# Performance work log

Hardware: AMD Instinct MI355X
Metric: run time of the kernel (lower is better)

Reference implementation:

```python
import jax, jax.numpy as jnp
import numpy as np

D_MODEL = 1024
ED = 2048        # d_inner = expand_factor * d_model
N = 16           # d_state
DT_RANK = 64     # ceil(d_model/16)
K = 4            # d_conv
B_SZ = 4
L = 512


def _causal_depthwise_conv(u, w, b):
    # u: [B, L, ED], w: [ED, 1, K], b: [ED]
    xc = jnp.transpose(u, (0, 2, 1))  # [B, ED, L]
    xc = jax.lax.conv_general_dilated(
        xc, w, window_strides=(1,), padding=[(K - 1, 0)],
        feature_group_count=ED, dimension_numbers=('NCH', 'OIH', 'NCH'))
    xc = xc + b[None, :, None]
    return jnp.transpose(xc, (0, 2, 1))  # [B, L, ED]


def _ssm_branch(xz_half, z, conv_w, conv_b, Wx, Wdt, b_dt, A_log, Dp):
    # xz_half, z: [B, L, ED]
    x = jax.nn.silu(_causal_depthwise_conv(xz_half, conv_w, conv_b))
    dbc = x @ Wx.T  # [B, L, dt_rank + 2N]
    delta = dbc[..., :DT_RANK]
    Bm = dbc[..., DT_RANK:DT_RANK + N]
    Cm = dbc[..., DT_RANK + N:]
    delta = jax.nn.softplus(delta @ Wdt.T + b_dt)  # [B, L, ED]
    A = -jnp.exp(A_log)  # [ED, N]
    dA = jnp.exp(delta[..., None] * A)                        # [B, L, ED, N]
    bx = (delta[..., None] * Bm[:, :, None, :]) * x[..., None]  # [B, L, ED, N]
    dA_t = jnp.transpose(dA, (1, 0, 2, 3))
    bx_t = jnp.transpose(bx, (1, 0, 2, 3))
    c_t = jnp.transpose(Cm, (1, 0, 2))  # [L, B, N]
    h0 = jnp.zeros((x.shape[0], ED, N), dtype=x.dtype)

    def step(h, inp):
        dAi, bxi, ci = inp
        h = dAi * h + bxi
        return h, jnp.einsum('ben,bn->be', h, ci)

    _, ys = jax.lax.scan(step, h0, (dA_t, bx_t, c_t))
    y = jnp.transpose(ys, (1, 0, 2)) + Dp * x  # D skip connection
    return y * jax.nn.silu(z)                  # gate


def _mamba_block(x, W_in, conv_w, conv_b, Wx, Wdt, b_dt, A_log, Dp,
                 conv_w_b, conv_b_b, Wx_b, Wdt_b, b_dt_b, A_log_b, Dp_b, W_out):
    xz = x @ W_in.T  # [B, L, 2*ED]
    xf, zf = xz[..., :ED], xz[..., ED:]
    y = _ssm_branch(xf, zf, conv_w, conv_b, Wx, Wdt, b_dt, A_log, Dp)
    xz_r = xz[:, ::-1, :]
    xb, zb = xz_r[..., :ED], xz_r[..., ED:]
    y_b = _ssm_branch(xb, zb, conv_w_b, conv_b_b, Wx_b, Wdt_b, b_dt_b, A_log_b, Dp_b)
    y = (y + y_b[:, ::-1, :]) * 0.5
    return y @ W_out.T


def setup_inputs() -> dict:
    key = jax.random.key(0)
    ks = jax.random.split(key, 20)
    s = lambda k, shp, sc: jax.random.normal(k, shp, dtype=jnp.float32) * sc
    dt = jnp.exp(jax.random.uniform(ks[15], (ED,)) * (np.log(0.1) - np.log(0.001)) + np.log(0.001))
    dt = jnp.clip(dt, 1e-4, None)
    inv_dt = dt + jnp.log(-jnp.expm1(-dt))
    A_init = jnp.log(jnp.tile(jnp.arange(1, N + 1, dtype=jnp.float32), (ED, 1)))
    return {
        'x': s(ks[0], (B_SZ, L, D_MODEL), 1.0),
        'W_in': s(ks[1], (2 * ED, D_MODEL), D_MODEL ** -0.5),
        'conv_w': s(ks[2], (ED, 1, K), K ** -0.5),
        'conv_b': s(ks[3], (ED,), 0.02),
        'Wx': s(ks[4], (DT_RANK + 2 * N, ED), ED ** -0.5),
        'Wdt': jax.random.uniform(ks[5], (ED, DT_RANK), minval=-DT_RANK ** -0.5, maxval=DT_RANK ** -0.5),
        'b_dt': inv_dt,
        'A_log': A_init,
        'Dp': jnp.ones((ED,), dtype=jnp.float32),
        'conv_w_b': s(ks[6], (ED, 1, K), K ** -0.5),
        'conv_b_b': s(ks[7], (ED,), 0.02),
        'Wx_b': s(ks[8], (DT_RANK + 2 * N, ED), ED ** -0.5),
        'Wdt_b': jax.random.uniform(ks[9], (ED, DT_RANK), minval=-DT_RANK ** -0.5, maxval=DT_RANK ** -0.5),
        'b_dt_b': inv_dt,
        'A_log_b': A_init,
        'Dp_b': jnp.ones((ED,), dtype=jnp.float32),
        'W_out': s(ks[10], (D_MODEL, ED), ED ** -0.5),
    }


def reference(x, W_in, conv_w, conv_b, Wx, Wdt, b_dt, A_log, Dp,
              conv_w_b, conv_b_b, Wx_b, Wdt_b, b_dt_b, A_log_b, Dp_b, W_out):
    return _mamba_block(x, W_in, conv_w, conv_b, Wx, Wdt, b_dt, A_log, Dp,
                        conv_w_b, conv_b_b, Wx_b, Wdt_b, b_dt_b, A_log_b, Dp_b, W_out)
```

## Files before the change

kernel.cpp:

```cpp
#include <hip/hip_runtime.h>
#include <hip/hip_bf16.h>
#include <stdint.h>

typedef unsigned short ushort_t;
typedef __attribute__((ext_vector_type(8))) short short8;
typedef __attribute__((ext_vector_type(4))) float f32x4;
typedef __attribute__((ext_vector_type(2))) float f32x2;

__device__ __forceinline__ float b2f(ushort_t u) {
    union { uint32_t i; float f; } v; v.i = ((uint32_t)u) << 16; return v.f;
}
__device__ __forceinline__ ushort_t f2b(float f) {
    union { float f; uint32_t i; } v; v.f = f;
    uint32_t r = v.i + 0x7fff + ((v.i >> 16) & 1);
    return (ushort_t)(r >> 16);
}

#if __has_builtin(__builtin_amdgcn_exp2f)
#define EXP2(x) __builtin_amdgcn_exp2f(x)
#else
#define EXP2(x) __expf((x) * 0.69314718056f)
#endif

__device__ __forceinline__ void ll16(const ushort_t* g, ushort_t* l) {
    __builtin_amdgcn_global_load_lds(
        (const __attribute__((address_space(1))) uint32_t*)g,
        (__attribute__((address_space(3))) uint32_t*)l, 16, 0, 0);
}

template <int CTRL>
__device__ __forceinline__ float dpp_add(float p) {
    int v = __builtin_amdgcn_update_dpp(0, __float_as_int(p), CTRL, 0xF, 0xF, true);
    return p + __int_as_float(v);
}
#define DPP_XOR1 0xB1
#define DPP_XOR2 0x4E
#define DPP_HMIR 0x141

__device__ __forceinline__ void epi_wave_f32(
    float* sw, const f32x4* accg, float* dst0, int ldc, int lane)
{
    const int quad = lane >> 4, lr = lane & 15;
#pragma unroll
    for (int j = 0; j < 4; j++)
#pragma unroll
        for (int r = 0; r < 4; r++)
            sw[(quad * 4 + r) * 64 + j * 16 + lr] = accg[j][r];
    __asm__ volatile("s_waitcnt lgkmcnt(0)" ::: "memory");
#pragma unroll
    for (int t = 0; t < 4; t++) {
        int row = t * 4 + quad;
        float4 v = *(const float4*)(&sw[row * 64 + lr * 4]);
        *(float4*)(dst0 + (size_t)row * ldc + lr * 4) = v;
    }
}

__device__ __forceinline__ void epi_wave_b16(
    float* sw, const f32x4* accg, ushort_t* dst0, int ldc, int lane)
{
    const int quad = lane >> 4, lr = lane & 15;
#pragma unroll
    for (int j = 0; j < 4; j++)
#pragma unroll
        for (int r = 0; r < 4; r++)
            sw[(quad * 4 + r) * 64 + j * 16 + lr] = accg[j][r];
    __asm__ volatile("s_waitcnt lgkmcnt(0)" ::: "memory");
#pragma unroll
    for (int t = 0; t < 4; t++) {
        int row = t * 4 + quad;
        float4 v = *(const float4*)(&sw[row * 64 + lr * 4]);
        ushort4 o; o.x = f2b(v.x); o.y = f2b(v.y); o.z = f2b(v.z); o.w = f2b(v.w);
        *(ushort4*)(dst0 + (size_t)row * ldc + lr * 4) = o;
    }
}

struct CastSeg { const float4* src; ushort4* dst; };
struct CastArgs { CastSeg seg[7]; int start[8]; };

__global__ __launch_bounds__(256) void cast_multi(CastArgs a)
{
    int g = blockIdx.x * 256 + threadIdx.x;
    if (g >= a.start[7]) return;
    int s = 0;
#pragma unroll
    for (int i = 1; i < 7; i++) s += (g >= a.start[i]);
    int i = g - a.start[s];
    float4 v = a.seg[s].src[i];
    ushort4 o;
    o.x = f2b(v.x); o.y = f2b(v.y); o.z = f2b(v.z); o.w = f2b(v.w);
    a.seg[s].dst[i] = o;
}

#define BK 32

__global__ __launch_bounds__(256) void gemm_g1(
    const ushort_t* __restrict__ A, int lda,
    const ushort_t* __restrict__ B, int ldb,
    ushort_t* __restrict__ Cout, int ldc, int Kd)
{
    __shared__ ushort_t As[2][128 * BK];
    __shared__ ushort_t Bs[2][128 * BK];
    __shared__ float sepi[4][1024];

    const int tid  = threadIdx.x;
    const int m0   = blockIdx.y * 128;
    const int n0   = blockIdx.x * 128;
    const int wv   = tid >> 6;
    const int lane = tid & 63;
    const int wm   = (wv >> 1) * 64;
    const int wn   = (wv & 1) * 64;
    const int lr   = lane & 15;
    const int quad = lane >> 4;

    f32x4 acc[4][4];
#pragma unroll
    for (int i = 0; i < 4; i++)
#pragma unroll
        for (int j = 0; j < 4; j++) acc[i][j] = f32x4{0.f, 0.f, 0.f, 0.f};

    const int srA = wv * 32 + (lane >> 2);
    const int scA = (lane & 3) * 8;

    auto stage = [&](int bf_, int k0) {
        ll16(A + (size_t)(m0 + srA) * lda + k0 + scA,      &As[bf_][wv * 1024]);
        ll16(A + (size_t)(m0 + srA + 16) * lda + k0 + scA, &As[bf_][wv * 1024 + 512]);
        ll16(B + (size_t)(n0 + srA) * ldb + k0 + scA,      &Bs[bf_][wv * 1024]);
        ll16(B + (size_t)(n0 + srA + 16) * ldb + k0 + scA, &Bs[bf_][wv * 1024 + 512]);
    };

    const int nk = Kd / BK;
    stage(0, 0);
    __syncthreads();

    for (int t = 0; t < nk; ++t) {
        const int buf = t & 1;
        if (t + 1 < nk) stage(buf ^ 1, (t + 1) * BK);

        short8 af[4], bfr[4];
#pragma unroll
        for (int i = 0; i < 4; i++)
            af[i] = *(const short8*)(&As[buf][(wm + i * 16 + lr) * BK + quad * 8]);
#pragma unroll
        for (int j = 0; j < 4; j++)
            bfr[j] = *(const short8*)(&Bs[buf][(wn + j * 16 + lr) * BK + quad * 8]);
#pragma unroll
        for (int i = 0; i < 4; i++)
#pragma unroll
            for (int j = 0; j < 4; j++)
                acc[i][j] = __builtin_amdgcn_mfma_f32_16x16x32_bf16(af[i], bfr[j], acc[i][j], 0, 0, 0);
        __syncthreads();
    }

#pragma unroll
    for (int g = 0; g < 4; g++)
        epi_wave_b16(sepi[wv], acc[g],
                     Cout + (size_t)(m0 + wm + g * 16) * ldc + n0 + wn, ldc, lane);
}

__global__ __launch_bounds__(256) void gemm_g4(
    const ushort_t* __restrict__ yfp, const ushort_t* __restrict__ ybp,
    const ushort_t* __restrict__ B, int ldb,
    float* __restrict__ part)
{
    __shared__ ushort_t As[2][64 * BK];
    __shared__ ushort_t Bs[2][128 * BK];
    __shared__ float sepi[4][1024];

    const int tid  = threadIdx.x;
    const int m0   = blockIdx.y * 64;
    const int n0   = blockIdx.x * 128;
    const int kz   = blockIdx.z;
    const int kbase = kz * 1024;
    const int wv   = tid >> 6;
    const int lane = tid & 63;
    const int wm   = (wv >> 1) * 32;
    const int wn   = (wv & 1) * 64;
    const int lr   = lane & 15;
    const int quad = lane >> 4;

    f32x4 acc[2][4];
#pragma unroll
    for (int i = 0; i < 2; i++)
#pragma unroll
        for (int j = 0; j < 4; j++) acc[i][j] = f32x4{0.f, 0.f, 0.f, 0.f};

    const int srA = wv * 16 + (lane >> 2);
    const int srB = wv * 32 + (lane >> 2);
    const int sc  = (lane & 3) * 8;

    const int arow = m0 + srA;
    const int t_   = arow & 511;
    const size_t yf_off = (size_t)arow * 2048;
    const size_t yb_off = (size_t)(arow - t_ + 511 - t_) * 2048;

    uint4 ra, rb;
    auto loadA = [&](int k0) {
        ra = *(const uint4*)(yfp + yf_off + kbase + k0 + sc);
        rb = *(const uint4*)(ybp + yb_off + kbase + k0 + sc);
    };
    auto writeA = [&](int bf_) {
        const uint32_t pa[4] = { ra.x, ra.y, ra.z, ra.w };
        const uint32_t pb[4] = { rb.x, rb.y, rb.z, rb.w };
        uint32_t w[4];
#pragma unroll
        for (int k = 0; k < 4; k++) {
            float a0 = b2f((ushort_t)(pa[k] & 0xffff));
            float a1 = b2f((ushort_t)(pa[k] >> 16));
            float c0 = b2f((ushort_t)(pb[k] & 0xffff));
            float c1 = b2f((ushort_t)(pb[k] >> 16));
            w[k] = (uint32_t)f2b(0.5f * (a0 + c0)) |
                   ((uint32_t)f2b(0.5f * (a1 + c1)) << 16);
        }
        *(uint4*)(&As[bf_][wv * 512 + (lane >> 2) * 32 + (lane & 3) * 8]) =
            make_uint4(w[0], w[1], w[2], w[3]);
    };
    auto stageB = [&](int bf_, int k0) {
        ll16(B + (size_t)(n0 + srB) * ldb + kbase + k0 + sc,      &Bs[bf_][wv * 1024]);
        ll16(B + (size_t)(n0 + srB + 16) * ldb + kbase + k0 + sc, &Bs[bf_][wv * 1024 + 512]);
    };

    const int nk = 1024 / BK;
    loadA(0);
    stageB(0, 0);
    writeA(0);
    __syncthreads();

    for (int t = 0; t < nk; ++t) {
        const int buf = t & 1;
        if (t + 1 < nk) {
            loadA((t + 1) * BK);
            stageB(buf ^ 1, (t + 1) * BK);
        }

        short8 af[2], bfr[4];
#pragma unroll
        for (int i = 0; i < 2; i++)
            af[i] = *(const short8*)(&As[buf][(wm + i * 16 + lr) * BK + quad * 8]);
#pragma unroll
        for (int j = 0; j < 4; j++)
            bfr[j] = *(const short8*)(&Bs[buf][(wn + j * 16 + lr) * BK + quad * 8]);
#pragma unroll
        for (int i = 0; i < 2; i++)
#pragma unroll
            for (int j = 0; j < 4; j++)
                acc[i][j] = __builtin_amdgcn_mfma_f32_16x16x32_bf16(af[i], bfr[j], acc[i][j], 0, 0, 0);

        if (t + 1 < nk) writeA(buf ^ 1);
        __syncthreads();
    }

    float* Cout = part + (size_t)kz * 2048 * 1024;
#pragma unroll
    for (int g = 0; g < 2; g++)
        epi_wave_f32(sepi[wv], acc[g],
                     Cout + (size_t)(m0 + wm + g * 16) * 1024 + n0 + wn, 1024, lane);
}

__global__ __launch_bounds__(256) void reduce_g4(
    const float4* __restrict__ part, float4* __restrict__ out)
{
    int g = blockIdx.x * 256 + threadIdx.x;
    const int S = 2048 * 1024 / 4;
    float4 a = part[g], b = part[g + S];
    float4 o; o.x = a.x + b.x; o.y = a.y + b.y; o.z = a.z + b.z; o.w = a.w + b.w;
    out[g] = o;
}

__global__ __launch_bounds__(256) void gemm_g2(
    const ushort_t* __restrict__ xc, const ushort_t* __restrict__ wx,
    float* __restrict__ part)
{
    __shared__ ushort_t As[2][128 * BK];
    __shared__ ushort_t Bs[2][128 * BK];
    __shared__ float sepi[4][1024];

    const int sk = blockIdx.x, mb = blockIdx.y, br = blockIdx.z;
    const ushort_t* A = xc + (size_t)br * 2048 * 2048;
    const ushort_t* B = wx + (size_t)br * 96 * 2048;
    float* C = part + (size_t)(sk * 2 + br) * 2048 * 96;
    const int m0 = mb * 128;
    const int kb = sk * 256;

    const int tid  = threadIdx.x;
    const int wv   = tid >> 6;
    const int lane = tid & 63;
    const int wm   = (wv >> 1) * 64;
    const int wn   = (wv & 1) * 64;
    const int lr   = lane & 15;
    const int quad = lane >> 4;

    f32x4 acc[4][4];
#pragma unroll
    for (int i = 0; i < 4; i++)
#pragma unroll
        for (int j = 0; j < 4; j++) acc[i][j] = f32x4{0.f, 0.f, 0.f, 0.f};

    const int srA = wv * 32 + (lane >> 2);
    const int sc  = (lane & 3) * 8;

    auto stage = [&](int bf_, int k0) {
        ll16(A + (size_t)(m0 + srA) * 2048 + k0 + sc,      &As[bf_][wv * 1024]);
        ll16(A + (size_t)(m0 + srA + 16) * 2048 + k0 + sc, &As[bf_][wv * 1024 + 512]);
        ll16(B + (size_t)(srA) * 2048 + k0 + sc,           &Bs[bf_][wv * 1024]);
        ll16(B + (size_t)(srA + 16) * 2048 + k0 + sc,      &Bs[bf_][wv * 1024 + 512]);
    };

    stage(0, kb);
    __syncthreads();

    for (int t = 0; t < 8; ++t) {
        const int buf = t & 1;
        if (t + 1 < 8) stage(buf ^ 1, kb + (t + 1) * BK);

        short8 af[4], bfr[4];
#pragma unroll
        for (int i = 0; i < 4; i++)
            af[i] = *(const short8*)(&As[buf][(wm + i * 16 + lr) * BK + quad * 8]);
#pragma unroll
        for (int j = 0; j < 4; j++)
            bfr[j] = *(const short8*)(&Bs[buf][(wn + j * 16 + lr) * BK + quad * 8]);
#pragma unroll
        for (int i = 0; i < 4; i++)
#pragma unroll
            for (int j = 0; j < 4; j++)
                acc[i][j] = __builtin_amdgcn_mfma_f32_16x16x32_bf16(af[i], bfr[j], acc[i][j], 0, 0, 0);
        __syncthreads();
    }

    float* sw = sepi[wv];
#pragma unroll
    for (int g = 0; g < 4; g++) {
#pragma unroll
        for (int j = 0; j < 4; j++)
#pragma unroll
            for (int r = 0; r < 4; r++)
                sw[(quad * 4 + r) * 64 + j * 16 + lr] = acc[g][j][r];
        __asm__ volatile("s_waitcnt lgkmcnt(0)" ::: "memory");
        int col = wn + lr * 4;
#pragma unroll
        for (int t = 0; t < 4; t++) {
            int row = t * 4 + quad;
            if (col < 96) {
                float4 v = *(const float4*)(&sw[row * 64 + lr * 4]);
                *(float4*)(C + (size_t)(m0 + wm + g * 16 + row) * 96 + col) = v;
            }
        }
    }
}

__global__ __launch_bounds__(256) void reduce_dbc(
    const float4* __restrict__ part, ushort4* __restrict__ dbc16)
{
    int g = blockIdx.x * 256 + threadIdx.x;
    const int S = 2 * 2048 * 96 / 4;
    float4 r = part[g];
#pragma unroll
    for (int i = 1; i < 8; i++) {
        float4 p = part[g + i * S];
        r.x += p.x; r.y += p.y; r.z += p.z; r.w += p.w;
    }
    ushort4 o; o.x = f2b(r.x); o.y = f2b(r.y); o.z = f2b(r.z); o.w = f2b(r.w);
    dbc16[g] = o;
}

__global__ __launch_bounds__(256) void gemm_g3(
    const ushort_t* __restrict__ dbc16, const ushort_t* __restrict__ wdt,
    ushort_t* __restrict__ delta,
    const float* __restrict__ bdt_f, const float* __restrict__ bdt_b)
{
    __shared__ ushort_t As[2][128 * BK];
    __shared__ ushort_t Bs[2][128 * BK];
    __shared__ float sepi[4][1024];

    const int br = blockIdx.z;
    const ushort_t* A = dbc16 + (size_t)br * 2048 * 96;
    const ushort_t* B = wdt + (size_t)br * 2048 * 64;
    ushort_t* C = delta + (size_t)br * 2048 * 2048;
    const float* bias = br ? bdt_b : bdt_f;

    const int tid  = threadIdx.x;
    const int m0   = blockIdx.y * 128;
    const int n0   = blockIdx.x * 128;
    const int wv   = tid >> 6;
    const int lane = tid & 63;
    const int wm   = (wv >> 1) * 64;
    const int wn   = (wv & 1) * 64;
    const int lr   = lane & 15;
    const int quad = lane >> 4;

    f32x4 acc[4][4];
#pragma unroll
    for (int i = 0; i < 4; i++)
#pragma unroll
        for (int j = 0; j < 4; j++) acc[i][j] = f32x4{0.f, 0.f, 0.f, 0.f};

    const int srA = wv * 32 + (lane >> 2);
    const int sc  = (lane & 3) * 8;

    auto stage = [&](int bf_, int k0) {
        ll16(A + (size_t)(m0 + srA) * 96 + k0 + sc,       &As[bf_][wv * 1024]);
        ll16(A + (size_t)(m0 + srA + 16) * 96 + k0 + sc,  &As[bf_][wv * 1024 + 512]);
        ll16(B + (size_t)(n0 + srA) * 64 + k0 + sc,       &Bs[bf_][wv * 1024]);
        ll16(B + (size_t)(n0 + srA + 16) * 64 + k0 + sc,  &Bs[bf_][wv * 1024 + 512]);
    };

    stage(0, 0);
    __syncthreads();

    for (int t = 0; t < 2; ++t) {
        const int buf = t & 1;
        if (t + 1 < 2) stage(buf ^ 1, (t + 1) * BK);

        short8 af[4], bfr[4];
#pragma unroll
        for (int i = 0; i < 4; i++)
            af[i] = *(const short8*)(&As[buf][(wm + i * 16 + lr) * BK + quad * 8]);
#pragma unroll
        for (int j = 0; j < 4; j++)
            bfr[j] = *(const short8*)(&Bs[buf][(wn + j * 16 + lr) * BK + quad * 8]);
#pragma unroll
        for (int i = 0; i < 4; i++)
#pragma unroll
            for (int j = 0; j < 4; j++)
                acc[i][j] = __builtin_amdgcn_mfma_f32_16x16x32_bf16(af[i], bfr[j], acc[i][j], 0, 0, 0);
        __syncthreads();
    }

    float bn[4];
#pragma unroll
    for (int j = 0; j < 4; j++) bn[j] = bias[n0 + wn + j * 16 + lr];
#pragma unroll
    for (int g = 0; g < 4; g++)
#pragma unroll
        for (int j = 0; j < 4; j++)
#pragma unroll
            for (int r = 0; r < 4; r++) {
                float x = acc[g][j][r] + bn[j];
                float sp = fmaxf(x, 0.f) + __logf(1.f + __expf(-fabsf(x)));
                acc[g][j][r] = sp;
            }

#pragma unroll
    for (int g = 0; g < 4; g++)
        epi_wave_b16(sepi[wv], acc[g],
                     C + (size_t)(m0 + wm + g * 16) * 2048 + n0 + wn, 2048, lane);
}

__global__ __launch_bounds__(256) void conv_silu_kernel(
    const ushort_t* __restrict__ xz,
    const float* __restrict__ w_f, const float* __restrict__ cb_f,
    const float* __restrict__ w_b, const float* __restrict__ cb_b,
    ushort_t* __restrict__ xc16)
{
    int g = blockIdx.x * 256 + threadIdx.x;
    int e  = g & 2047;
    int t  = (g >> 11) & 511;
    int b  = (g >> 20) & 3;
    int br = g >> 22;

    const float* w  = br ? w_b  : w_f;
    const float* cb = br ? cb_b : cb_f;

    float acc = cb[e];
    float4 wv = *(const float4*)(w + e * 4);
    float wk[4] = { wv.x, wv.y, wv.z, wv.w };

#pragma unroll
    for (int k = 0; k < 4; k++) {
        int tp = t - 3 + k;
        if (tp >= 0) {
            int row = br ? (511 - tp) : tp;
            acc += wk[k] * b2f(xz[((size_t)(b * 512 + row)) * 4096 + e]);
        }
    }
    float s = acc / (1.f + __expf(-acc));
    xc16[g] = f2b(s);
}

__global__ __launch_bounds__(256, 4) void scan_kernel(
    const ushort_t* __restrict__ delta,
    const ushort_t* __restrict__ xc,
    const ushort_t* __restrict__ dbc16,
    const ushort_t* __restrict__ xz,
    const float* __restrict__ Alog_f, const float* __restrict__ Alog_b,
    const float* __restrict__ Dp_f,   const float* __restrict__ Dp_b,
    ushort_t* __restrict__ yf, ushort_t* __restrict__ yb)
{
    const int blk = blockIdx.x;
    const int eg = blk & 63;
    const int b  = (blk >> 6) & 3;
    const int br = blk >> 8;
    const int e0 = eg * 32;

    const int tid = threadIdx.x;
    const int n2  = tid & 7;
    const int el  = tid >> 3;
    const int e   = e0 + el;

    const float* Alog = br ? Alog_b : Alog_f;
    const float* Dpp  = br ? Dp_b   : Dp_f;
    f32x2 a01;
    a01.x = -__expf(Alog[e * 16 + n2]) * 1.44269504f;
    a01.y = -__expf(Alog[e * 16 + n2 + 8]) * 1.44269504f;

    size_t tb = ((size_t)br * 4 + b) * 512;
    const ushort_t* dlt  = delta + tb * 2048;
    const ushort_t* xcb  = xc    + tb * 2048;
    const ushort_t* dbcb = dbc16 + tb * 96;
    ushort_t* y = (br ? yb : yf) + (size_t)b * 512 * 2048;

    __shared__ float sd [2][32][36];
    __shared__ float sdx[2][32][36];
    __shared__ float sBp[2][8][34][2];
    __shared__ float sCp[2][8][34][2];
    __shared__ float sy [2][32][33];

    const int stt = tid >> 3;
    const int seg = tid & 7;
    const int sg4 = seg * 4;
    const int sdk = (seg & 3) * 8;

    float4 rD = *(const float4*)(Dpp + e0 + sg4);

    uint2 rdx, rx, rbc, rz;
    uint2 rx_c, rx_f, rz_c, rz_f;

    auto load_regs = [&](int c) {
        int row = c * 32 + stt;
        rdx = *(const uint2*)(dlt + (size_t)row * 2048 + e0 + sg4);
        rx  = *(const uint2*)(xcb + (size_t)row * 2048 + e0 + sg4);
        rbc = *(const uint2*)(dbcb + (size_t)row * 96 + 64 + sg4);
        int orow = br ? (511 - row) : row;
        rz  = *(const uint2*)(xz + ((size_t)(b * 512 + orow)) * 4096 + 2048 + e0 + sg4);
    };
    auto write_lds = [&](int buf) {
        const uint32_t dw[2] = { rdx.x, rdx.y };
        const uint32_t xw[2] = { rx.x, rx.y };
        const int col = stt ^ sdk;
#pragma unroll
        for (int k = 0; k < 2; k++) {
            float d0 = b2f((ushort_t)(dw[k] & 0xffff));
            float d1 = b2f((ushort_t)(dw[k] >> 16));
            float x0 = b2f((ushort_t)(xw[k] & 0xffff));
            float x1 = b2f((ushort_t)(xw[k] >> 16));
            sd [buf][sg4 + 2 * k][col]     = d0;
            sd [buf][sg4 + 2 * k + 1][col] = d1;
            sdx[buf][sg4 + 2 * k][col]     = d0 * x0;
            sdx[buf][sg4 + 2 * k + 1][col] = d1 * x1;
        }
        float* arr = (seg < 4) ? &sBp[buf][0][0][0] : &sCp[buf][0][0][0];
        const int nb = (seg & 3) * 4;
        const uint32_t bw[2] = { rbc.x, rbc.y };
#pragma unroll
        for (int k = 0; k < 2; k++) {
            int na = nb + 2 * k, nbd = nb + 2 * k + 1;
            arr[(na  & 7) * 68 + stt * 2 + (na  >> 3)] = b2f((ushort_t)(bw[k] & 0xffff));
            arr[(nbd & 7) * 68 + stt * 2 + (nbd >> 3)] = b2f((ushort_t)(bw[k] >> 16));
        }
    };
    auto flush = [&](int cm1) {
        const int bufm1 = cm1 & 1;
        int row = cm1 * 32 + stt;
        const uint32_t zw[2] = { rz_f.x, rz_f.y };
        float zv[4];
#pragma unroll
        for (int k = 0; k < 2; k++) {
            zv[2 * k]     = b2f((ushort_t)(zw[k] & 0xffff));
            zv[2 * k + 1] = b2f((ushort_t)(zw[k] >> 16));
        }
        float pv[4];
#pragma unroll
        for (int k = 0; k < 4; k++) pv[k] = sy[bufm1][stt][sg4 + k];
        const uint32_t xw[2] = { rx_f.x, rx_f.y };
        float xvv[4];
#pragma unroll
        for (int k = 0; k < 2; k++) {
            xvv[2 * k]     = b2f((ushort_t)(xw[k] & 0xffff));
            xvv[2 * k + 1] = b2f((ushort_t)(xw[k] >> 16));
        }
        const float Dv[4] = { rD.x, rD.y, rD.z, rD.w };
        uint32_t op[2];
#pragma unroll
        for (int k = 0; k < 2; k++) {
            float ga = (pv[2 * k]     + Dv[2 * k]     * xvv[2 * k])     *
                       (zv[2 * k]     / (1.f + __expf(-zv[2 * k])));
            float gb = (pv[2 * k + 1] + Dv[2 * k + 1] * xvv[2 * k + 1]) *
                       (zv[2 * k + 1] / (1.f + __expf(-zv[2 * k + 1])));
            op[k] = (uint32_t)f2b(ga) | ((uint32_t)f2b(gb) << 16);
        }
        *(uint2*)(y + (size_t)row * 2048 + e0 + sg4) = make_uint2(op[0], op[1]);
    };

    f32x2 h01 = f32x2{0.f, 0.f};
    const int elk = ((el >> 2) & 3) * 8;

    load_regs(0);
    write_lds(0);
    rx_c = rx; rz_c = rz;

    for (int c = 0; c < 16; ++c) {
        if (c < 15) load_regs(c + 1);
        __syncthreads();
        const int buf = c & 1;

        auto LDQ = [&](int tq, f32x4& dv, f32x4& dxv, f32x4& bq0, f32x4& bq1,
                       f32x4& cq0, f32x4& cq1) {
            const int tc = tq ^ elk;
            dv  = *(const f32x4*)(&sd [buf][el][tc]);
            dxv = *(const f32x4*)(&sdx[buf][el][tc]);
            bq0 = *(const f32x4*)(&sBp[buf][n2][tq][0]);
            bq1 = *(const f32x4*)(&sBp[buf][n2][tq + 2][0]);
            cq0 = *(const f32x4*)(&sCp[buf][n2][tq][0]);
            cq1 = *(const f32x4*)(&sCp[buf][n2][tq + 2][0]);
        };

        f32x4 dv_p, dxv_p, bq0_p, bq1_p, cq0_p, cq1_p;
        LDQ(0, dv_p, dxv_p, bq0_p, bq1_p, cq0_p, cq1_p);

        float pout[4];
#pragma unroll 4
        for (int tq = 0; tq < 32; tq += 4) {
            const f32x4 dv = dv_p, dxv = dxv_p;
            const f32x4 bq0 = bq0_p, bq1 = bq1_p, cq0 = cq0_p, cq1 = cq1_p;
            LDQ((tq + 4) & 31, dv_p, dxv_p, bq0_p, bq1_p, cq0_p, cq1_p);

#define SSTEP(DC, DXC, BT, CT, TI)                                   \
            {                                                        \
                f32x2 arg = a01 * (DC);                              \
                f32x2 ee; ee.x = EXP2(arg.x); ee.y = EXP2(arg.y);    \
                h01 = ee * h01 + (BT) * (DXC);                       \
                f32x2 pp = h01 * (CT);                               \
                float p = pp.x + pp.y;                               \
                p = dpp_add<DPP_XOR1>(p);                            \
                p = dpp_add<DPP_XOR2>(p);                            \
                p = dpp_add<DPP_HMIR>(p);                            \
                pout[TI] = p;                                        \
            }
            SSTEP(dv.x, dxv.x, bq0.xy, cq0.xy, 0)
            SSTEP(dv.y, dxv.y, bq0.zw, cq0.zw, 1)
            SSTEP(dv.z, dxv.z, bq1.xy, cq1.xy, 2)
            SSTEP(dv.w, dxv.w, bq1.zw, cq1.zw, 3)
#undef SSTEP

            if (n2 == 0) {
                sy[buf][tq + 0][el] = pout[0];
                sy[buf][tq + 1][el] = pout[1];
                sy[buf][tq + 2][el] = pout[2];
                sy[buf][tq + 3][el] = pout[3];
            }
        }

        if (c > 0) flush(c - 1);

        if (c < 15) {
            write_lds((c + 1) & 1);
            rx_f = rx_c; rz_f = rz_c;
            rx_c = rx;   rz_c = rz;
        } else {
            rx_f = rx_c; rz_f = rz_c;
        }
    }
    __syncthreads();
    flush(15);
}

static const size_t TT = 2048;
static const size_t OFF_XZ16  = 0;
static const size_t OFF_XC16  = OFF_XZ16  + TT*4096*2;
static const size_t OFF_DBC16 = OFF_XC16  + 2*TT*2048*2;
static const size_t OFF_DELTA = OFF_DBC16 + 2*TT*96*2;
static const size_t OFF_YF    = OFF_DELTA + 2*TT*2048*2;
static const size_t OFF_YB    = OFF_YF    + TT*2048*2;
static const size_t OFF_YC16  = OFF_YB    + TT*2048*2;
static const size_t OFF_X16   = OFF_YC16  + TT*2048*2;
static const size_t OFF_WIN16 = OFF_X16   + TT*1024*2;
static const size_t OFF_WX16  = OFF_WIN16 + 4096*1024*2;
static const size_t OFF_WDT16 = OFF_WX16  + 2*96*2048*2;
static const size_t OFF_WOUT16= OFF_WDT16 + 2*2048*64*2;
static const size_t OFF_PART  = OFF_WOUT16+ 1024*2048*2;

extern "C" void kernel_launch(void* const* d_in, const int* in_sizes, int n_in,
                              void* d_out, int out_size, void* d_ws, size_t ws_size,
                              hipStream_t stream) {
    const float* x       = (const float*)d_in[0];
    const float* W_in    = (const float*)d_in[1];
    const float* conv_w  = (const float*)d_in[2];
    const float* conv_b  = (const float*)d_in[3];
    const float* Wx      = (const float*)d_in[4];
    const float* Wdt     = (const float*)d_in[5];
    const float* b_dt    = (const float*)d_in[6];
    const float* A_log   = (const float*)d_in[7];
    const float* Dp      = (const float*)d_in[8];
    const float* conv_w_b= (const float*)d_in[9];
    const float* conv_b_b= (const float*)d_in[10];
    const float* Wx_b    = (const float*)d_in[11];
    const float* Wdt_b   = (const float*)d_in[12];
    const float* b_dt_b  = (const float*)d_in[13];
    const float* A_log_b = (const float*)d_in[14];
    const float* Dp_b    = (const float*)d_in[15];
    const float* W_out   = (const float*)d_in[16];
    float* out = (float*)d_out;

    char* ws = (char*)d_ws;
    ushort_t* xz16  = (ushort_t*)(ws + OFF_XZ16);
    ushort_t* xc16  = (ushort_t*)(ws + OFF_XC16);
    ushort_t* dbc16 = (ushort_t*)(ws + OFF_DBC16);
    ushort_t* delta = (ushort_t*)(ws + OFF_DELTA);
    ushort_t* yf    = (ushort_t*)(ws + OFF_YF);
    ushort_t* yb    = (ushort_t*)(ws + OFF_YB);
    ushort_t* x16   = (ushort_t*)(ws + OFF_X16);
    ushort_t* win16 = (ushort_t*)(ws + OFF_WIN16);
    ushort_t* wx16  = (ushort_t*)(ws + OFF_WX16);
    ushort_t* wdt16 = (ushort_t*)(ws + OFF_WDT16);
    ushort_t* wout16= (ushort_t*)(ws + OFF_WOUT16);
    float*    part  = (float*)(ws + OFF_PART);
    float*    part4 = (float*)(ws + OFF_DELTA);

    dim3 blk(256);

    CastArgs ca;
    const int n4s[7] = {524288, 1048576, 49152, 49152, 32768, 32768, 524288};
    ca.seg[0] = { (const float4*)x,     (ushort4*)x16 };
    ca.seg[1] = { (const float4*)W_in,  (ushort4*)win16 };
    ca.seg[2] = { (const float4*)Wx,    (ushort4*)wx16 };
    ca.seg[3] = { (const float4*)Wx_b,  (ushort4*)(wx16 + 96 * 2048) };
    ca.seg[4] = { (const float4*)Wdt,   (ushort4*)wdt16 };
    ca.seg[5] = { (const float4*)Wdt_b, (ushort4*)(wdt16 + 2048 * 64) };
    ca.seg[6] = { (const float4*)W_out, (ushort4*)wout16 };
    ca.start[0] = 0;
    for (int i = 0; i < 7; i++) ca.start[i + 1] = ca.start[i] + n4s[i];
    cast_multi<<<(ca.start[7] + 255) / 256, blk, 0, stream>>>(ca);

    gemm_g1<<<dim3(32, 16), blk, 0, stream>>>(x16, 1024, win16, 1024, xz16, 4096, 1024);

    conv_silu_kernel<<<32768, blk, 0, stream>>>(xz16, conv_w, conv_b, conv_w_b, conv_b_b, xc16);

    gemm_g2<<<dim3(8, 16, 2), blk, 0, stream>>>(xc16, wx16, part);
    reduce_dbc<<<384, blk, 0, stream>>>((const float4*)part, (ushort4*)dbc16);

    gemm_g3<<<dim3(16, 16, 2), blk, 0, stream>>>(dbc16, wdt16, delta, b_dt, b_dt_b);

    scan_kernel<<<512, blk, 0, stream>>>(delta, xc16, dbc16, xz16, A_log, A_log_b, Dp, Dp_b, yf, yb);

    gemm_g4<<<dim3(8, 32, 2), blk, 0, stream>>>(yf, yb, wout16, 2048, part4);
    reduce_g4<<<2048, blk, 0, stream>>>((const float4*)part4, (float4*)out);
}
```

Before: 266.6 us.

## Swizzle GEMM block order across XCDs and vectorize conv-silu to 8 channels

```diff
diff --git a/kernel.cpp b/kernel.cpp
--- a/kernel.cpp
+++ b/kernel.cpp
@@ -102,9 +102,12 @@
     __shared__ ushort_t Bs[2][128 * BK];
     __shared__ float sepi[4][1024];
 
+    const int flat = blockIdx.y * 32 + blockIdx.x;
+    const int swz  = (flat & 7) * 64 + (flat >> 3);
+    const int m0   = (swz >> 5) * 128;
+    const int n0   = (swz & 31) * 128;
+
     const int tid  = threadIdx.x;
-    const int m0   = blockIdx.y * 128;
-    const int n0   = blockIdx.x * 128;
     const int wv   = tid >> 6;
     const int lane = tid & 63;
     const int wm   = (wv >> 1) * 64;
@@ -166,10 +169,13 @@
     __shared__ ushort_t Bs[2][128 * BK];
     __shared__ float sepi[4][1024];
 
+    const int flat = (blockIdx.z * 32 + blockIdx.y) * 8 + blockIdx.x;
+    const int swz  = (flat & 7) * 64 + (flat >> 3);
+    const int n0   = (swz & 7) * 128;
+    const int m0   = ((swz >> 3) & 31) * 64;
+    const int kz   = swz >> 8;
+
     const int tid  = threadIdx.x;
-    const int m0   = blockIdx.y * 64;
-    const int n0   = blockIdx.x * 128;
-    const int kz   = blockIdx.z;
     const int kbase = kz * 1024;
     const int wv   = tid >> 6;
     const int lane = tid & 63;
@@ -274,7 +280,12 @@
     __shared__ ushort_t Bs[2][128 * BK];
     __shared__ float sepi[4][1024];
 
-    const int sk = blockIdx.x, mb = blockIdx.y, br = blockIdx.z;
+    const int flat = (blockIdx.z * 16 + blockIdx.y) * 8 + blockIdx.x;
+    const int swz  = (flat & 7) * 32 + (flat >> 3);
+    const int sk   = swz & 7;
+    const int mb   = (swz >> 3) & 15;
+    const int br   = swz >> 7;
+
     const ushort_t* A = xc + (size_t)br * 2048 * 2048;
     const ushort_t* B = wx + (size_t)br * 96 * 2048;
     float* C = part + (size_t)(sk * 2 + br) * 2048 * 96;
@@ -372,15 +383,18 @@
     __shared__ ushort_t Bs[2][128 * BK];
     __shared__ float sepi[4][1024];
 
-    const int br = blockIdx.z;
+    const int flat = (blockIdx.z * 16 + blockIdx.y) * 16 + blockIdx.x;
+    const int swz  = (flat & 7) * 64 + (flat >> 3);
+    const int n0   = (swz & 15) * 128;
+    const int m0   = ((swz >> 4) & 15) * 128;
+    const int br   = swz >> 8;
+
     const ushort_t* A = dbc16 + (size_t)br * 2048 * 96;
     const ushort_t* B = wdt + (size_t)br * 2048 * 64;
     ushort_t* C = delta + (size_t)br * 2048 * 2048;
     const float* bias = br ? bdt_b : bdt_f;
 
     const int tid  = threadIdx.x;
-    const int m0   = blockIdx.y * 128;
-    const int n0   = blockIdx.x * 128;
     const int wv   = tid >> 6;
     const int lane = tid & 63;
     const int wm   = (wv >> 1) * 64;
@@ -453,28 +467,52 @@
     ushort_t* __restrict__ xc16)
 {
     int g = blockIdx.x * 256 + threadIdx.x;
-    int e  = g & 2047;
-    int t  = (g >> 11) & 511;
-    int b  = (g >> 20) & 3;
-    int br = g >> 22;
+    int e0 = (g & 255) * 8;
+    int t  = (g >> 8) & 511;
+    int b  = (g >> 17) & 3;
+    int br = g >> 19;
 
     const float* w  = br ? w_b  : w_f;
     const float* cb = br ? cb_b : cb_f;
 
-    float acc = cb[e];
-    float4 wv = *(const float4*)(w + e * 4);
-    float wk[4] = { wv.x, wv.y, wv.z, wv.w };
-
+    uint32_t tv[4][4];
 #pragma unroll
     for (int k = 0; k < 4; k++) {
         int tp = t - 3 + k;
         if (tp >= 0) {
             int row = br ? (511 - tp) : tp;
-            acc += wk[k] * b2f(xz[((size_t)(b * 512 + row)) * 4096 + e]);
-        }
-    }
-    float s = acc / (1.f + __expf(-acc));
-    xc16[g] = f2b(s);
+            uint4 xv = *(const uint4*)(xz + ((size_t)(b * 512 + row)) * 4096 + e0);
+            tv[k][0] = xv.x; tv[k][1] = xv.y; tv[k][2] = xv.z; tv[k][3] = xv.w;
+        } else {
+            tv[k][0] = 0; tv[k][1] = 0; tv[k][2] = 0; tv[k][3] = 0;
+        }
+    }
+
+    float4 cbv0 = *(const float4*)(cb + e0);
+    float4 cbv1 = *(const float4*)(cb + e0 + 4);
+    const float cbs[8] = { cbv0.x, cbv0.y, cbv0.z, cbv0.w,
+                           cbv1.x, cbv1.y, cbv1.z, cbv1.w };
+
+    uint32_t op[4];
+#pragma unroll
+    for (int q = 0; q < 4; q++) {
+        float4 wA = *(const float4*)(w + (e0 + 2 * q) * 4);
+        float4 wB = *(const float4*)(w + (e0 + 2 * q + 1) * 4);
+        float a0 = cbs[2 * q]
+                 + wA.x * b2f((ushort_t)(tv[0][q] & 0xffff))
+                 + wA.y * b2f((ushort_t)(tv[1][q] & 0xffff))
+                 + wA.z * b2f((ushort_t)(tv[2][q] & 0xffff))
+                 + wA.w * b2f((ushort_t)(tv[3][q] & 0xffff));
+        float a1 = cbs[2 * q + 1]
+                 + wB.x * b2f((ushort_t)(tv[0][q] >> 16))
+                 + wB.y * b2f((ushort_t)(tv[1][q] >> 16))
+                 + wB.z * b2f((ushort_t)(tv[2][q] >> 16))
+                 + wB.w * b2f((ushort_t)(tv[3][q] >> 16));
+        float s0 = a0 / (1.f + __expf(-a0));
+        float s1 = a1 / (1.f + __expf(-a1));
+        op[q] = (uint32_t)f2b(s0) | ((uint32_t)f2b(s1) << 16);
+    }
+    *(uint4*)(xc16 + (size_t)g * 8) = make_uint4(op[0], op[1], op[2], op[3]);
 }
 
 __global__ __launch_bounds__(256, 4) void scan_kernel(
@@ -733,7 +771,7 @@
 
     gemm_g1<<<dim3(32, 16), blk, 0, stream>>>(x16, 1024, win16, 1024, xz16, 4096, 1024);
 
-    conv_silu_kernel<<<32768, blk, 0, stream>>>(xz16, conv_w, conv_b, conv_w_b, conv_b_b, xc16);
+    conv_silu_kernel<<<4096, blk, 0, stream>>>(xz16, conv_w, conv_b, conv_w_b, conv_b_b, xc16);
 
     gemm_g2<<<dim3(8, 16, 2), blk, 0, stream>>>(xc16, wx16, part);
     reduce_dbc<<<384, blk, 0, stream>>>((const float4*)part, (ushort4*)dbc16);
```

New measurement: 261.8 us. Within noise of the previous version (-1.8%).
